# Kernel tuning notes

Measured on AMD Instinct MI355X. Metric: run time of the kernel, lower is better.

The kernel has to match this reference:

```python
import jax, jax.numpy as jnp
import numpy as np

NU, NB, NI = 50000, 20000, 100000
D = 64
NUM_LAYERS = 2
CORE_K = 3
PAD = NI  # padding index for bundle_items
BATCH, NCAND = 2048, 2
MAXDEG = 50
E_UB, E_UI, E_BI = 800000, 1000000, 1200000
N_UB, N_UI, N_BI = NU + NB, NU + NI, NB + NI


def setup_inputs():
    key = jax.random.key(0)
    ks = jax.random.split(key, 24)
    f = jnp.float32
    inp = {
        'users_feature': jax.random.normal(ks[0], (NU, D), f) * 0.1,
        'bundles_feature': jax.random.normal(ks[1], (NB, D), f) * 0.1,
        'items_feature': jax.random.normal(ks[2], (NI, D), f) * 0.1,
        'mlp_core_w1': jax.random.normal(ks[3], (2, 32), f) * 0.1,
        'mlp_core_b1': jnp.zeros((32,), f),
        'mlp_core_w2': jax.random.normal(ks[4], (32, 1), f) * 0.1,
        'mlp_core_b2': jnp.zeros((1,), f),
        'mlp_syn_w1': jax.random.normal(ks[5], (2 * D, D), f) * 0.05,
        'mlp_syn_b1': jnp.zeros((D,), f),
        'mlp_syn_w2': jax.random.normal(ks[6], (D, D), f) * 0.05,
        'mlp_syn_b2': jnp.zeros((D,), f),
        'ub_val': jax.random.uniform(ks[7], (E_UB,), f) * 0.2,
        'ui_val': jax.random.uniform(ks[8], (E_UI,), f) * 0.2,
        'bi_val': jax.random.uniform(ks[9], (E_BI,), f) * 0.2,
        'users': jax.random.randint(ks[10], (BATCH,), 0, NU),
        'bundles': jax.random.randint(ks[11], (BATCH, NCAND), 0, NB),
        'ub_row': jax.random.randint(ks[12], (E_UB,), 0, N_UB, jnp.int32),
        'ub_col': jax.random.randint(ks[13], (E_UB,), 0, N_UB, jnp.int32),
        'ui_row': jax.random.randint(ks[14], (E_UI,), 0, N_UI, jnp.int32),
        'ui_col': jax.random.randint(ks[15], (E_UI,), 0, N_UI, jnp.int32),
        'bi_row': jax.random.randint(ks[16], (E_BI,), 0, N_BI, jnp.int32),
        'bi_col': jax.random.randint(ks[17], (E_BI,), 0, N_BI, jnp.int32),
        'bundle_items': jax.random.randint(ks[18], (NB, MAXDEG), 0, NI + 1),
    }
    return inp


def spmm(row, col, val, x):
    # y = A @ x for COO sparse A: gather source rows, scale, scatter-add to dest rows
    return jax.ops.segment_sum(val[:, None] * x[col], row, num_segments=x.shape[0])


def propagate(row, col, val, feat_a, feat_b):
    f = jnp.concatenate([feat_a, feat_b], axis=0)
    acc = f
    for _ in range(NUM_LAYERS):
        f = spmm(row, col, val, f)
        acc = acc + f
    m = acc / (NUM_LAYERS + 1)  # mean over hop outputs
    return m[:feat_a.shape[0]], m[feat_a.shape[0]:]


def core_fringe_scores(users, bundles, reps, bundle_items,
                       cw1, cb1, cw2, cb2, sw1, sb1, sw2, sb2):
    UB_u, UB_b, UI_u, UI_i, BI_b, BI_i = reps
    B, C = bundles.shape
    users_exp = jnp.repeat(users, C)            # [B*C]
    bundles_flat = bundles.reshape(-1)          # [B*C]
    bbi = bundle_items[bundles_flat]            # [B*C, M]
    mask = bbi != PAD
    zero = jnp.zeros((1, D), UI_i.dtype)
    items_ui = jnp.concatenate([UI_i, zero], 0)[bbi]  # [B*C, M, D]
    items_bi = jnp.concatenate([BI_i, zero], 0)[bbi]
    u_ui = UI_u[users_exp]                      # [B*C, D]
    b_bi = BI_b[bundles_flat]
    r_UI = jnp.einsum('nd,nmd->nm', u_ui, items_ui)
    r_BI = jnp.einsum('nd,nmd->nm', b_bi, items_bi)
    x = jnp.stack([r_UI, r_BI], axis=-1)        # [B*C, M, 2]
    h = jax.nn.relu(x @ cw1 + cb1)              # dropout omitted (eval-mode determinism)
    logits = (h @ cw2 + cb2)[..., 0]
    logits = jnp.where(mask, logits, -jnp.inf)
    pi = jax.nn.softmax(logits, axis=1)
    k = min(CORE_K, bbi.shape[1])
    topv, topi = jax.lax.top_k(pi, k)
    topp = topv / (topv.sum(axis=1, keepdims=True) + 1e-10)
    core_emb = jnp.take_along_axis(items_ui, topi[:, :, None], axis=1)
    h_core = (core_emb * topp[:, :, None]).sum(axis=1)
    n = pi.shape[0]
    is_core = jnp.zeros(pi.shape, bool).at[jnp.arange(n)[:, None], topi].set(True)
    is_fringe = mask & ~is_core
    fr = is_fringe[:, :, None].astype(items_ui.dtype)
    fringe_sum = (items_ui * fr).sum(axis=1)
    fringe_cnt = jnp.maximum(is_fringe.sum(axis=1, keepdims=True).astype(items_ui.dtype), 1.0)
    h_fringe = fringe_sum / fringe_cnt
    syn = jnp.concatenate([h_core, h_fringe], axis=1)
    phi = jax.nn.relu(syn @ sw1 + sb1) @ sw2 + sb2
    hat_e_BI = h_core + phi
    user_final = jnp.concatenate([u_ui, UB_u[users_exp]], axis=1)
    bundle_final = jnp.concatenate([UB_b[bundles_flat], hat_e_BI], axis=1)
    scores = (user_final * bundle_final).sum(axis=1)
    return scores.reshape(B, C)


def reference(users_feature, bundles_feature, items_feature,
              mlp_core_w1, mlp_core_b1, mlp_core_w2, mlp_core_b2,
              mlp_syn_w1, mlp_syn_b1, mlp_syn_w2, mlp_syn_b2,
              ub_val, ui_val, bi_val,
              users, bundles, ub_row, ub_col, ui_row, ui_col,
              bi_row, bi_col, bundle_items):
    UB_u, UB_b = propagate(ub_row, ub_col, ub_val, users_feature, bundles_feature)
    UI_u, UI_i = propagate(ui_row, ui_col, ui_val, users_feature, items_feature)
    BI_b, BI_i = propagate(bi_row, bi_col, bi_val, bundles_feature, items_feature)
    reps = (UB_u, UB_b, UI_u, UI_i, BI_b, BI_i)
    scores = core_fringe_scores(users, bundles, reps, bundle_items,
                                mlp_core_w1, mlp_core_b1, mlp_core_w2, mlp_core_b2,
                                mlp_syn_w1, mlp_syn_b1, mlp_syn_w2, mlp_syn_b2)
    # BPR loss: -log(sigmoid(pos - neg)) == softplus(neg - pos)
    bpr_loss = jnp.mean(jax.nn.softplus(scores[:, 1:] - scores[:, 0:1]))
    return bpr_loss
```

## Files before the change

### kernel.cpp

```cpp
#include <hip/hip_runtime.h>
#include <math.h>

constexpr int D = 64;
constexpr int NU = 50000, NB = 20000, NI = 100000;
constexpr int BATCH = 2048, NCAND = 2, MAXDEG = 50, CORE_K = 3;
constexpr int PAD_IDX = NI;
constexpr int N_UB = NU + NB, N_UI = NU + NI, N_BI = NB + NI;
constexpr int N_TOT = N_UB + N_UI + N_BI;
constexpr int OFF1 = N_UB;
constexpr int OFF2 = N_UB + N_UI;
constexpr int CAP = 48;
constexpr float VAL_SCALE = 16383.0f / 0.2f;
constexpr float VAL_INV   = 0.2f / 16383.0f;

constexpr int GB_BASE = NU;
constexpr int GI_BASE = NU + NB;
constexpr int NGF = NU + NB + NI;

constexpr int BSHIFT = 11;
constexpr int BROWS  = 1 << BSHIFT;
constexpr int NBUCK  = (N_TOT + BROWS - 1) >> BSHIFT;
constexpr int BCAP   = 24576;
constexpr int P1_EPT = 16;
constexpr int P1_TPB = 256;
constexpr int P1_EPB = P1_EPT * P1_TPB;
constexpr int SPLIT  = 4;
constexpr int RWIN   = BROWS / SPLIT;

constexpr int L2_NCB = BATCH * NCAND;
constexpr int L2_SLOTS = 2 * NI + 2 * BATCH + 2 * L2_NCB;
constexpr int S_UBU = 2 * NI;
constexpr int S_UIU = 2 * NI + BATCH;
constexpr int S_UBB = 2 * NI + 2 * BATCH;
constexpr int S_BIB = S_UBB + L2_NCB;

__device__ __forceinline__ float wave_sum64(float v) {
#pragma unroll
    for (int off = 32; off > 0; off >>= 1) v += __shfl_down(v, off);
    return v;
}

__device__ __forceinline__ float bflo(unsigned u) { return __uint_as_float(u << 16); }
__device__ __forceinline__ float bfhi(unsigned u) { return __uint_as_float(u & 0xFFFF0000u); }
__device__ __forceinline__ unsigned short f2bf(float f) {
    unsigned u = __float_as_uint(f);
    u += 0x7FFF + ((u >> 16) & 1);
    return (unsigned short)(u >> 16);
}
__device__ __forceinline__ unsigned pack2(float a, float b) {
    return (unsigned)f2bf(a) | ((unsigned)f2bf(b) << 16);
}
__device__ __forceinline__ float bf1(const unsigned short* p) {
    return __uint_as_float(((unsigned)*p) << 16);
}

__device__ __forceinline__ void edge_decode(unsigned u, int& col, float& v) {
    col = (int)(u & 0x3FFFFu);
    v = (float)(u >> 18) * VAL_INV;
}

__device__ __forceinline__ void gather_rows(const unsigned* __restrict__ ce, int deg,
                                            const unsigned short* __restrict__ src,
                                            int t8, float a[8]) {
    int j = 0;
    for (; j + 3 < deg; j += 4) {
        int c[4]; float v[4]; uint4 u[4];
#pragma unroll
        for (int k = 0; k < 4; ++k) edge_decode(ce[j + k], c[k], v[k]);
#pragma unroll
        for (int k = 0; k < 4; ++k)
            u[k] = *(const uint4*)(src + (((size_t)c[k]) << 6) + t8 * 8);
#pragma unroll
        for (int k = 0; k < 4; ++k) {
            a[0] = fmaf(v[k], bflo(u[k].x), a[0]); a[1] = fmaf(v[k], bfhi(u[k].x), a[1]);
            a[2] = fmaf(v[k], bflo(u[k].y), a[2]); a[3] = fmaf(v[k], bfhi(u[k].y), a[3]);
            a[4] = fmaf(v[k], bflo(u[k].z), a[4]); a[5] = fmaf(v[k], bfhi(u[k].z), a[5]);
            a[6] = fmaf(v[k], bflo(u[k].w), a[6]); a[7] = fmaf(v[k], bfhi(u[k].w), a[7]);
        }
    }
    for (; j < deg; ++j) {
        int c0; float v0;
        edge_decode(ce[j], c0, v0);
        uint4 u0 = *(const uint4*)(src + (((size_t)c0) << 6) + t8 * 8);
        a[0] = fmaf(v0, bflo(u0.x), a[0]); a[1] = fmaf(v0, bfhi(u0.x), a[1]);
        a[2] = fmaf(v0, bflo(u0.y), a[2]); a[3] = fmaf(v0, bfhi(u0.y), a[3]);
        a[4] = fmaf(v0, bflo(u0.z), a[4]); a[5] = fmaf(v0, bfhi(u0.z), a[5]);
        a[6] = fmaf(v0, bflo(u0.w), a[6]); a[7] = fmaf(v0, bfhi(u0.w), a[7]);
    }
}

__global__ __launch_bounds__(256) void k_bin1cvt(
    const int* __restrict__ r0, const int* __restrict__ c0,
    const float* __restrict__ v0,
    const int* __restrict__ r1, const int* __restrict__ c1,
    const float* __restrict__ v1,
    const int* __restrict__ r2, const int* __restrict__ c2,
    const float* __restrict__ v2,
    int e0, int e1, int e2, int nb1,
    int* __restrict__ bcnt, uint2* __restrict__ stage,
    const float* __restrict__ uf, const float* __restrict__ bf,
    const float* __restrict__ itf, unsigned short* __restrict__ gt) {
    const int t = threadIdx.x;
    if ((int)blockIdx.x >= nb1) {
        size_t i = (size_t)(blockIdx.x - nb1) * 256 + t;
        if (i >= (size_t)NGF * 16) return;
        int row = (int)(i >> 4);
        int q = ((int)i & 15) * 4;
        const float* src;
        if (row < GB_BASE)      src = uf  + (size_t)row * D;
        else if (row < GI_BASE) src = bf  + (size_t)(row - GB_BASE) * D;
        else                    src = itf + (size_t)(row - GI_BASE) * D;
        float4 v = *(const float4*)(src + q);
        ushort4 o;
        o.x = f2bf(v.x); o.y = f2bf(v.y); o.z = f2bf(v.z); o.w = f2bf(v.w);
        *(ushort4*)(gt + (size_t)row * D + q) = o;
        return;
    }
    __shared__ int s_hist[NBUCK];
    __shared__ unsigned s_base[NBUCK];
    const int etot = e0 + e1 + e2;
    const int i0 = blockIdx.x * P1_EPB + t;
    if (t < NBUCK) s_hist[t] = 0;
    __syncthreads();
    unsigned el[P1_EPT], er[P1_EPT];
#pragma unroll
    for (int k = 0; k < P1_EPT; ++k) {
        int i = i0 + k * P1_TPB;
        if (i < etot) {
            int r, g; float v;
            if (i < e0)           { r = r0[i]; g = c0[i]; v = v0[i]; }
            else if (i < e0 + e1) { int j = i - e0; r = r1[j] + OFF1;
                                    int c = c1[j]; g = (c < NU) ? c : c + NB; v = v1[j]; }
            else                  { int j = i - e0 - e1; r = r2[j] + OFF2;
                                    g = c2[j] + NU; v = v2[j]; }
            unsigned q = (unsigned)fminf(v * VAL_SCALE + 0.5f, 16383.0f);
            el[k] = (q << 18) | (unsigned)g;
            int lo = atomicAdd(&s_hist[r >> BSHIFT], 1);
            er[k] = (unsigned)r | ((unsigned)lo << 19);
        } else {
            er[k] = 0xFFFFFFFFu;
        }
    }
    __syncthreads();
    if (t < NBUCK) s_base[t] = (unsigned)atomicAdd(&bcnt[t], s_hist[t]);
    __syncthreads();
#pragma unroll
    for (int k = 0; k < P1_EPT; ++k) {
        unsigned eh = er[k];
        if (eh == 0xFFFFFFFFu) continue;
        unsigned r = eh & 0x7FFFFu;
        unsigned b = r >> BSHIFT;
        unsigned slot = s_base[b] + (eh >> 19);
        if (slot < (unsigned)BCAP)
            stage[(size_t)b * BCAP + slot] = make_uint2(el[k], r);
    }
}

__global__ __launch_bounds__(512) void k_bin2l1(
    const int* __restrict__ bcnt, const uint2* __restrict__ stage,
    const unsigned short* __restrict__ gt,
    int* __restrict__ cnt, unsigned* __restrict__ cv,
    unsigned short* __restrict__ y1) {
    __shared__ int s_c[RWIN];
    const int cb = blockIdx.x >> 2;
    const int p  = blockIdx.x & 3;
    const int t  = threadIdx.x;
    const int rb = (cb << BSHIFT) + p * RWIN;
    s_c[t] = 0;
    __syncthreads();
    int nb = bcnt[cb]; if (nb > BCAP) nb = BCAP;
    const uint2* sp = stage + (size_t)cb * BCAP;
    for (int i = t; i < nb; i += 512) {
        uint2 e = sp[i];
        int rl = (int)e.y - rb;
        if ((unsigned)rl < (unsigned)RWIN) {
            int slot = atomicAdd(&s_c[rl], 1);
            if (slot < CAP) cv[(size_t)e.y * CAP + slot] = e.x;
        }
    }
    __syncthreads();
    if (rb + t < N_TOT) cnt[rb + t] = s_c[t];
    const int t8 = t & 7;
#pragma unroll 1
    for (int pass = 0; pass < 8; ++pass) {
        int rl = pass * 64 + (t >> 3);
        int r = rb + rl;
        if (r >= N_TOT) continue;
        int deg = s_c[rl]; if (deg > CAP) deg = CAP;
        float a[8];
#pragma unroll
        for (int k = 0; k < 8; ++k) a[k] = 0.f;
        gather_rows(cv + (size_t)r * CAP, deg, gt, t8, a);
        uint4 o;
        o.x = pack2(a[0], a[1]); o.y = pack2(a[2], a[3]);
        o.z = pack2(a[4], a[5]); o.w = pack2(a[6], a[7]);
        *(uint4*)(y1 + ((size_t)r << 6) + t8 * 8) = o;
    }
}

__global__ __launch_bounds__(256) void k_spmm_l2(
    const int* __restrict__ cnt, const unsigned* __restrict__ cv,
    const int* __restrict__ users, const int* __restrict__ bundles,
    const unsigned short* __restrict__ y1, const unsigned short* __restrict__ gt,
    unsigned short* __restrict__ xc) {
    int s = blockIdx.x * 32 + (threadIdx.x >> 3);
    int t = threadIdx.x & 7;
    if (s >= L2_SLOTS) return;
    int r, g, sec;
    if (s < NI)                { r = OFF1 + NU + s;        g = GI_BASE + s;        sec = 1; }
    else if (s < 2 * NI)       { int i = s - NI;
                                 r = OFF2 + NB + i;        g = GI_BASE + i;        sec = 2; }
    else {
        int q = s - 2 * NI;
        if (q < BATCH)            { int u = users[q];             r = u;         g = u;            sec = 0; }
        else if (q < 2 * BATCH)   { int u = users[q - BATCH];     r = OFF1 + u;  g = u;            sec = 1; }
        else if (q < S_BIB - 2 * NI) { int b = bundles[q - 2 * BATCH];
                                    r = NU + b;    g = GB_BASE + b;  sec = 0; }
        else                      { int b = bundles[q - (S_BIB - 2 * NI)];
                                    r = OFF2 + b;  g = GB_BASE + b;  sec = 2; }
    }
    auto y1row = [&](int gg) -> int {
        if (sec == 0) return gg;
        if (sec == 2) return OFF2 - GB_BASE + gg;
        return OFF1 + ((gg < NU) ? gg : gg - NB);
    };
    int deg = cnt[r]; if (deg > CAP) deg = CAP;
    const unsigned* ce = cv + (size_t)r * CAP;
    float a[8];
#pragma unroll
    for (int k = 0; k < 8; ++k) a[k] = 0.f;
    int j = 0;
    for (; j + 3 < deg; j += 4) {
        int c[4]; float v[4]; uint4 u[4];
#pragma unroll
        for (int k = 0; k < 4; ++k) edge_decode(ce[j + k], c[k], v[k]);
#pragma unroll
        for (int k = 0; k < 4; ++k)
            u[k] = *(const uint4*)(y1 + (((size_t)y1row(c[k])) << 6) + t * 8);
#pragma unroll
        for (int k = 0; k < 4; ++k) {
            a[0] = fmaf(v[k], bflo(u[k].x), a[0]); a[1] = fmaf(v[k], bfhi(u[k].x), a[1]);
            a[2] = fmaf(v[k], bflo(u[k].y), a[2]); a[3] = fmaf(v[k], bfhi(u[k].y), a[3]);
            a[4] = fmaf(v[k], bflo(u[k].z), a[4]); a[5] = fmaf(v[k], bfhi(u[k].z), a[5]);
            a[6] = fmaf(v[k], bflo(u[k].w), a[6]); a[7] = fmaf(v[k], bfhi(u[k].w), a[7]);
        }
    }
    for (; j < deg; ++j) {
        int c0; float v0;
        edge_decode(ce[j], c0, v0);
        uint4 u0 = *(const uint4*)(y1 + (((size_t)y1row(c0)) << 6) + t * 8);
        a[0] = fmaf(v0, bflo(u0.x), a[0]); a[1] = fmaf(v0, bfhi(u0.x), a[1]);
        a[2] = fmaf(v0, bflo(u0.y), a[2]); a[3] = fmaf(v0, bfhi(u0.y), a[3]);
        a[4] = fmaf(v0, bflo(u0.z), a[4]); a[5] = fmaf(v0, bfhi(u0.z), a[5]);
        a[6] = fmaf(v0, bflo(u0.w), a[6]); a[7] = fmaf(v0, bfhi(u0.w), a[7]);
    }
    uint4 fx = *(const uint4*)(gt + ((size_t)g << 6) + t * 8);
    uint4 yx = *(const uint4*)(y1 + ((size_t)r << 6) + t * 8);
    constexpr float k3 = 1.0f / 3.0f;
    float o[8];
    o[0] = (bflo(fx.x) + bflo(yx.x) + a[0]) * k3;
    o[1] = (bfhi(fx.x) + bfhi(yx.x) + a[1]) * k3;
    o[2] = (bflo(fx.y) + bflo(yx.y) + a[2]) * k3;
    o[3] = (bfhi(fx.y) + bfhi(yx.y) + a[3]) * k3;
    o[4] = (bflo(fx.z) + bflo(yx.z) + a[4]) * k3;
    o[5] = (bfhi(fx.z) + bfhi(yx.z) + a[5]) * k3;
    o[6] = (bflo(fx.w) + bflo(yx.w) + a[6]) * k3;
    o[7] = (bfhi(fx.w) + bfhi(yx.w) + a[7]) * k3;
    uint4 w;
    w.x = pack2(o[0], o[1]); w.y = pack2(o[2], o[3]);
    w.z = pack2(o[4], o[5]); w.w = pack2(o[6], o[7]);
    *(uint4*)(xc + ((size_t)s << 6) + t * 8) = w;
}

__global__ __launch_bounds__(256) void k_score(
    const int* __restrict__ bundles,
    const int* __restrict__ bundle_items,
    const unsigned short* __restrict__ xc,
    const float* __restrict__ cw1, const float* __restrict__ cb1,
    const float* __restrict__ cw2, const float* __restrict__ cb2,
    const float* __restrict__ sw1, const float* __restrict__ sb1,
    const float* __restrict__ sw2, const float* __restrict__ sb2,
    float* __restrict__ accum, unsigned* __restrict__ tick,
    float* __restrict__ out) {
    const int t  = threadIdx.x;
    const int wv = t >> 6;
    const int ln = t & 63;
    const int n  = blockIdx.x * 4 + wv;
    const int g8 = ln >> 3;
    const int l8 = ln & 7;
    const int uq = n >> 1;
    const int b = bundles[n];

    __shared__ unsigned sh_it[4][MAXDEG][32];
    __shared__ float sh_r[4][2][MAXDEG];
    __shared__ float sh_syn[4][2 * D];
    __shared__ float sh_h1[4][D];
    __shared__ float sh_sc[4];

    int my_idx = (ln < MAXDEG) ? bundle_items[(size_t)b * MAXDEG + ln] : PAD_IDX;
    unsigned long long vmask = __ballot(my_idx != PAD_IDX);

    uint4 ufr = *(const uint4*)(xc + (((size_t)(S_UIU + uq)) << 6) + l8 * 8);
    uint4 bfr = *(const uint4*)(xc + (((size_t)(S_BIB + n)) << 6) + l8 * 8);
    float uf0 = bflo(ufr.x), uf1 = bfhi(ufr.x), uf2 = bflo(ufr.y), uf3 = bfhi(ufr.y);
    float uf4 = bflo(ufr.z), uf5 = bfhi(ufr.z), uf6 = bflo(ufr.w), uf7 = bfhi(ufr.w);
    float bf0 = bflo(bfr.x), bf1_ = bfhi(bfr.x), bf2 = bflo(bfr.y), bf3 = bfhi(bfr.y);
    float bf4 = bflo(bfr.z), bf5 = bfhi(bfr.z), bf6 = bflo(bfr.w), bf7 = bfhi(bfr.w);

    for (int iter = 0; iter < (MAXDEG + 7) / 8; ++iter) {
        int m = iter * 8 + g8;
        if (m >= MAXDEG) continue;
        int it = __shfl(my_idx, m);
        uint4 iu = make_uint4(0, 0, 0, 0);
        float pu = 0.f, pb = 0.f;
        if (it != PAD_IDX) {
            iu = *(const uint4*)(xc + (((size_t)it) << 6) + l8 * 8);
            uint4 ib = *(const uint4*)(xc + (((size_t)(NI + it)) << 6) + l8 * 8);
            pu = uf0 * bflo(iu.x) + uf1 * bfhi(iu.x) + uf2 * bflo(iu.y) + uf3 * bfhi(iu.y)
               + uf4 * bflo(iu.z) + uf5 * bfhi(iu.z) + uf6 * bflo(iu.w) + uf7 * bfhi(iu.w);
            pb = bf0 * bflo(ib.x) + bf1_ * bfhi(ib.x) + bf2 * bflo(ib.y) + bf3 * bfhi(ib.y)
               + bf4 * bflo(ib.z) + bf5 * bfhi(ib.z) + bf6 * bflo(ib.w) + bf7 * bfhi(ib.w);
        }
        *(uint4*)&sh_it[wv][m][l8 * 4] = iu;
#pragma unroll
        for (int off = 4; off > 0; off >>= 1) {
            pu += __shfl_down(pu, off, 8);
            pb += __shfl_down(pb, off, 8);
        }
        if (l8 == 0) { sh_r[wv][0][m] = pu; sh_r[wv][1][m] = pb; }
    }
    __builtin_amdgcn_wave_barrier();

    float logit = -INFINITY;
    if (ln < MAXDEG && my_idx != PAD_IDX) {
        float rU = sh_r[wv][0][ln], rB = sh_r[wv][1][ln];
        float acc = cb2[0];
#pragma unroll
        for (int j = 0; j < 32; ++j) {
            float h = fmaf(rU, cw1[j], fmaf(rB, cw1[32 + j], cb1[j]));
            h = fmaxf(h, 0.f);
            acc = fmaf(h, cw2[j], acc);
        }
        logit = acc;
    }

    float mx = logit;
#pragma unroll
    for (int off = 32; off > 0; off >>= 1) mx = fmaxf(mx, __shfl_xor(mx, off));
    float e = expf(logit - mx);
    float sm = e;
#pragma unroll
    for (int off = 32; off > 0; off >>= 1) sm += __shfl_xor(sm, off);
    float p = e / sm;

    int ti[CORE_K]; float tp[CORE_K];
    float vsel = p;
#pragma unroll
    for (int k = 0; k < CORE_K; ++k) {
        float vv = vsel; int ii = ln;
#pragma unroll
        for (int off = 32; off > 0; off >>= 1) {
            float v2 = __shfl_xor(vv, off);
            int   i2 = __shfl_xor(ii, off);
            if (v2 > vv || (v2 == vv && i2 < ii)) { vv = v2; ii = i2; }
        }
        ti[k] = ii; tp[k] = vv;
        if (ln == ii) vsel = -1.f;
    }
    float tinv = 1.f / (tp[0] + tp[1] + tp[2] + 1e-10f);
    tp[0] *= tinv; tp[1] *= tinv; tp[2] *= tinv;

    int ti0 = ti[0], ti1 = ti[1], ti2 = ti[2];
    const int ui_w = ln >> 1;
    const bool hi = (ln & 1);
    auto feat = [&](int m) -> float {
        unsigned w = sh_it[wv][m][ui_w];
        return hi ? bfhi(w) : bflo(w);
    };
    float hcore = feat(ti0) * tp[0] + feat(ti1) * tp[1] + feat(ti2) * tp[2];
    float fsum = 0.f;
#pragma unroll 10
    for (int m = 0; m < MAXDEG; ++m) fsum += feat(m);
    int fcnt = __popcll(vmask);
#pragma unroll
    for (int k = 0; k < CORE_K; ++k) {
        if ((vmask >> ti[k]) & 1ull) { fsum -= feat(ti[k]); fcnt--; }
    }
    float hfr = fsum / fmaxf((float)fcnt, 1.f);
    sh_syn[wv][ln] = hcore;
    sh_syn[wv][D + ln] = hfr;
    __builtin_amdgcn_wave_barrier();

    float h1 = sb1[ln];
#pragma unroll 8
    for (int k0 = 0; k0 < 32; ++k0) {
        float4 s4 = *(const float4*)&sh_syn[wv][k0 * 4];
        h1 = fmaf(s4.x, sw1[(k0 * 4 + 0) * D + ln], h1);
        h1 = fmaf(s4.y, sw1[(k0 * 4 + 1) * D + ln], h1);
        h1 = fmaf(s4.z, sw1[(k0 * 4 + 2) * D + ln], h1);
        h1 = fmaf(s4.w, sw1[(k0 * 4 + 3) * D + ln], h1);
    }
    sh_h1[wv][ln] = fmaxf(h1, 0.f);
    __builtin_amdgcn_wave_barrier();
    float phi = sb2[ln];
#pragma unroll 8
    for (int k0 = 0; k0 < 16; ++k0) {
        float4 s4 = *(const float4*)&sh_h1[wv][k0 * 4];
        phi = fmaf(s4.x, sw2[(k0 * 4 + 0) * D + ln], phi);
        phi = fmaf(s4.y, sw2[(k0 * 4 + 1) * D + ln], phi);
        phi = fmaf(s4.z, sw2[(k0 * 4 + 2) * D + ln], phi);
        phi = fmaf(s4.w, sw2[(k0 * 4 + 3) * D + ln], phi);
    }

    float hat = hcore + phi;
    float uui = bf1(xc + (((size_t)(S_UIU + uq)) << 6) + ln);
    float ubu = bf1(xc + (((size_t)(S_UBU + uq)) << 6) + ln);
    float ubb = bf1(xc + (((size_t)(S_UBB + n)) << 6) + ln);
    float part = wave_sum64(uui * ubb + ubu * hat);
    if (ln == 0) sh_sc[wv] = part;

    __syncthreads();
    if (t == 0) {
        float x01 = sh_sc[1] - sh_sc[0];
        float x23 = sh_sc[3] - sh_sc[2];
        float spv = fmaxf(x01, 0.f) + log1pf(expf(-fabsf(x01)))
                  + fmaxf(x23, 0.f) + log1pf(expf(-fabsf(x23)));
        atomicAdd(accum, spv * (1.0f / (float)BATCH));
        __threadfence();
        unsigned old = atomicAdd(tick, 1u);
        if (old == gridDim.x - 1) {
            __threadfence();
            float total = atomicAdd(accum, 0.0f);
            out[0] = total;
        }
    }
}

extern "C" void kernel_launch(void* const* d_in, const int* in_sizes, int n_in,
                              void* d_out, int out_size, void* d_ws, size_t ws_size,
                              hipStream_t stream) {
    const float* users_feature   = (const float*)d_in[0];
    const float* bundles_feature = (const float*)d_in[1];
    const float* items_feature   = (const float*)d_in[2];
    const float* cw1 = (const float*)d_in[3];
    const float* cb1 = (const float*)d_in[4];
    const float* cw2 = (const float*)d_in[5];
    const float* cb2 = (const float*)d_in[6];
    const float* sw1 = (const float*)d_in[7];
    const float* sb1 = (const float*)d_in[8];
    const float* sw2 = (const float*)d_in[9];
    const float* sb2 = (const float*)d_in[10];
    const float* ub_val = (const float*)d_in[11];
    const float* ui_val = (const float*)d_in[12];
    const float* bi_val = (const float*)d_in[13];
    const int* users   = (const int*)d_in[14];
    const int* bundles = (const int*)d_in[15];
    const int* ub_row = (const int*)d_in[16];
    const int* ub_col = (const int*)d_in[17];
    const int* ui_row = (const int*)d_in[18];
    const int* ui_col = (const int*)d_in[19];
    const int* bi_row = (const int*)d_in[20];
    const int* bi_col = (const int*)d_in[21];
    const int* bundle_items = (const int*)d_in[22];
    const int E_UB = in_sizes[11], E_UI = in_sizes[12], E_BI = in_sizes[13];
    const int E_TOT = E_UB + E_UI + E_BI;

    float* ws = (float*)d_ws;
    size_t off = 0;
    unsigned short* gt  = (unsigned short*)(ws + off); off += (size_t)NGF * 32;
    unsigned short* y1b = (unsigned short*)(ws + off); off += (size_t)N_TOT * 32;
    unsigned* cv  = (unsigned*)(ws + off); off += (size_t)N_TOT * CAP;
    uint2* stage = (uint2*)(ws + off);
    unsigned short* xc = (unsigned short*)(ws + off);
    off += (size_t)NBUCK * BCAP * 2;
    int*   cnt    = (int*)(ws + off); off += N_TOT;
    int*   bcnt   = (int*)(ws + off); off += NBUCK;
    unsigned* tick = (unsigned*)(ws + off); off += 1;
    float* accum  = (float*)(ws + off); off += 1;
    if (ws_size < off * sizeof(float)) return;

    hipMemsetAsync(bcnt, 0, (NBUCK + 2) * sizeof(int), stream);

    const int nb1 = (E_TOT + P1_EPB - 1) / P1_EPB;
    const int ncvt = (int)(((size_t)NGF * 16 + 255) / 256);
    k_bin1cvt<<<nb1 + ncvt, P1_TPB, 0, stream>>>(
        ub_row, ub_col, ub_val, ui_row, ui_col, ui_val, bi_row, bi_col, bi_val,
        E_UB, E_UI, E_BI, nb1, bcnt, stage,
        users_feature, bundles_feature, items_feature, gt);

    k_bin2l1<<<NBUCK * SPLIT, 512, 0, stream>>>(bcnt, stage, gt, cnt, cv, y1b);

    k_spmm_l2<<<(L2_SLOTS + 31) / 32, 256, 0, stream>>>(
        cnt, cv, users, bundles, y1b, gt, xc);

    k_score<<<(BATCH * NCAND) / 4, 256, 0, stream>>>(
        bundles, bundle_items, xc,
        cw1, cb1, cw2, cb2, sw1, sb1, sw2, sb2,
        accum, tick, (float*)d_out);
}
```

Baseline: 381.4 us.

## Split bucket scatter from layer-1 SpMM and halve bucket size

Separates the second binning pass from the first-layer SpMM gather into two kernels. Binning now uses one block per bucket of 1024 rows, so each staged edge is read once instead of by four split blocks. The layer-1 SpMM runs as its own row-parallel kernel with many more blocks, which should improve latency hiding for the gathers. The cost is an extra kernel launch and re-reading cnt from global memory. More buckets also mean more global atomics in the first pass.

```diff
diff --git a/kernel.cpp b/kernel.cpp
--- a/kernel.cpp
+++ b/kernel.cpp
@@ -17,15 +17,13 @@
 constexpr int GI_BASE = NU + NB;
 constexpr int NGF = NU + NB + NI;
 
-constexpr int BSHIFT = 11;
+constexpr int BSHIFT = 10;
 constexpr int BROWS  = 1 << BSHIFT;
 constexpr int NBUCK  = (N_TOT + BROWS - 1) >> BSHIFT;
-constexpr int BCAP   = 24576;
+constexpr int BCAP   = 12288;
 constexpr int P1_EPT = 16;
 constexpr int P1_TPB = 256;
 constexpr int P1_EPB = P1_EPT * P1_TPB;
-constexpr int SPLIT  = 4;
-constexpr int RWIN   = BROWS / SPLIT;
 
 constexpr int L2_NCB = BATCH * NCAND;
 constexpr int L2_SLOTS = 2 * NI + 2 * BATCH + 2 * L2_NCB;
@@ -57,36 +55,6 @@
 __device__ __forceinline__ void edge_decode(unsigned u, int& col, float& v) {
     col = (int)(u & 0x3FFFFu);
     v = (float)(u >> 18) * VAL_INV;
-}
-
-__device__ __forceinline__ void gather_rows(const unsigned* __restrict__ ce, int deg,
-                                            const unsigned short* __restrict__ src,
-                                            int t8, float a[8]) {
-    int j = 0;
-    for (; j + 3 < deg; j += 4) {
-        int c[4]; float v[4]; uint4 u[4];
-#pragma unroll
-        for (int k = 0; k < 4; ++k) edge_decode(ce[j + k], c[k], v[k]);
-#pragma unroll
-        for (int k = 0; k < 4; ++k)
-            u[k] = *(const uint4*)(src + (((size_t)c[k]) << 6) + t8 * 8);
-#pragma unroll
-        for (int k = 0; k < 4; ++k) {
-            a[0] = fmaf(v[k], bflo(u[k].x), a[0]); a[1] = fmaf(v[k], bfhi(u[k].x), a[1]);
-            a[2] = fmaf(v[k], bflo(u[k].y), a[2]); a[3] = fmaf(v[k], bfhi(u[k].y), a[3]);
-            a[4] = fmaf(v[k], bflo(u[k].z), a[4]); a[5] = fmaf(v[k], bfhi(u[k].z), a[5]);
-            a[6] = fmaf(v[k], bflo(u[k].w), a[6]); a[7] = fmaf(v[k], bfhi(u[k].w), a[7]);
-        }
-    }
-    for (; j < deg; ++j) {
-        int c0; float v0;
-        edge_decode(ce[j], c0, v0);
-        uint4 u0 = *(const uint4*)(src + (((size_t)c0) << 6) + t8 * 8);
-        a[0] = fmaf(v0, bflo(u0.x), a[0]); a[1] = fmaf(v0, bfhi(u0.x), a[1]);
-        a[2] = fmaf(v0, bflo(u0.y), a[2]); a[3] = fmaf(v0, bfhi(u0.y), a[3]);
-        a[4] = fmaf(v0, bflo(u0.z), a[4]); a[5] = fmaf(v0, bfhi(u0.z), a[5]);
-        a[6] = fmaf(v0, bflo(u0.w), a[6]); a[7] = fmaf(v0, bfhi(u0.w), a[7]);
-    }
 }
 
 __global__ __launch_bounds__(256) void k_bin1cvt(
@@ -120,7 +88,7 @@
     __shared__ unsigned s_base[NBUCK];
     const int etot = e0 + e1 + e2;
     const int i0 = blockIdx.x * P1_EPB + t;
-    if (t < NBUCK) s_hist[t] = 0;
+    for (int l = t; l < NBUCK; l += P1_TPB) s_hist[l] = 0;
     __syncthreads();
     unsigned el[P1_EPT], er[P1_EPT];
 #pragma unroll
@@ -142,7 +110,8 @@
         }
     }
     __syncthreads();
-    if (t < NBUCK) s_base[t] = (unsigned)atomicAdd(&bcnt[t], s_hist[t]);
+    for (int l = t; l < NBUCK; l += P1_TPB)
+        s_base[l] = (unsigned)atomicAdd(&bcnt[l], s_hist[l]);
     __syncthreads();
 #pragma unroll
     for (int k = 0; k < P1_EPT; ++k) {
@@ -156,46 +125,69 @@
     }
 }
 
-__global__ __launch_bounds__(512) void k_bin2l1(
+__global__ __launch_bounds__(512) void k_bin2(
     const int* __restrict__ bcnt, const uint2* __restrict__ stage,
-    const unsigned short* __restrict__ gt,
-    int* __restrict__ cnt, unsigned* __restrict__ cv,
-    unsigned short* __restrict__ y1) {
-    __shared__ int s_c[RWIN];
-    const int cb = blockIdx.x >> 2;
-    const int p  = blockIdx.x & 3;
-    const int t  = threadIdx.x;
-    const int rb = (cb << BSHIFT) + p * RWIN;
-    s_c[t] = 0;
-    __syncthreads();
-    int nb = bcnt[cb]; if (nb > BCAP) nb = BCAP;
-    const uint2* sp = stage + (size_t)cb * BCAP;
+    int* __restrict__ cnt, unsigned* __restrict__ cv) {
+    __shared__ int s_c[BROWS];
+    const int b = blockIdx.x;
+    const int t = threadIdx.x;
+    for (int l = t; l < BROWS; l += 512) s_c[l] = 0;
+    __syncthreads();
+    int nb = bcnt[b]; if (nb > BCAP) nb = BCAP;
+    const uint2* sp = stage + (size_t)b * BCAP;
+    const int rbase = b << BSHIFT;
     for (int i = t; i < nb; i += 512) {
         uint2 e = sp[i];
-        int rl = (int)e.y - rb;
-        if ((unsigned)rl < (unsigned)RWIN) {
-            int slot = atomicAdd(&s_c[rl], 1);
-            if (slot < CAP) cv[(size_t)e.y * CAP + slot] = e.x;
-        }
-    }
-    __syncthreads();
-    if (rb + t < N_TOT) cnt[rb + t] = s_c[t];
-    const int t8 = t & 7;
-#pragma unroll 1
-    for (int pass = 0; pass < 8; ++pass) {
-        int rl = pass * 64 + (t >> 3);
-        int r = rb + rl;
-        if (r >= N_TOT) continue;
-        int deg = s_c[rl]; if (deg > CAP) deg = CAP;
-        float a[8];
-#pragma unroll
-        for (int k = 0; k < 8; ++k) a[k] = 0.f;
-        gather_rows(cv + (size_t)r * CAP, deg, gt, t8, a);
-        uint4 o;
-        o.x = pack2(a[0], a[1]); o.y = pack2(a[2], a[3]);
-        o.z = pack2(a[4], a[5]); o.w = pack2(a[6], a[7]);
-        *(uint4*)(y1 + ((size_t)r << 6) + t8 * 8) = o;
-    }
+        int slot = atomicAdd(&s_c[(int)e.y - rbase], 1);
+        if (slot < CAP) cv[(size_t)e.y * CAP + slot] = e.x;
+    }
+    __syncthreads();
+    for (int l = t; l < BROWS; l += 512) {
+        int r = rbase + l;
+        if (r < N_TOT) cnt[r] = s_c[l];
+    }
+}
+
+__global__ __launch_bounds__(256) void k_spmm_l1(
+    const int* __restrict__ cnt, const unsigned* __restrict__ cv,
+    const unsigned short* __restrict__ gt, unsigned short* __restrict__ y1) {
+    int r = blockIdx.x * 32 + (threadIdx.x >> 3);
+    int t = threadIdx.x & 7;
+    if (r >= N_TOT) return;
+    int deg = cnt[r]; if (deg > CAP) deg = CAP;
+    const unsigned* ce = cv + (size_t)r * CAP;
+    float a[8];
+#pragma unroll
+    for (int k = 0; k < 8; ++k) a[k] = 0.f;
+    int j = 0;
+    for (; j + 3 < deg; j += 4) {
+        int c[4]; float v[4]; uint4 u[4];
+#pragma unroll
+        for (int k = 0; k < 4; ++k) edge_decode(ce[j + k], c[k], v[k]);
+#pragma unroll
+        for (int k = 0; k < 4; ++k)
+            u[k] = *(const uint4*)(gt + (((size_t)c[k]) << 6) + t * 8);
+#pragma unroll
+        for (int k = 0; k < 4; ++k) {
+            a[0] = fmaf(v[k], bflo(u[k].x), a[0]); a[1] = fmaf(v[k], bfhi(u[k].x), a[1]);
+            a[2] = fmaf(v[k], bflo(u[k].y), a[2]); a[3] = fmaf(v[k], bfhi(u[k].y), a[3]);
+            a[4] = fmaf(v[k], bflo(u[k].z), a[4]); a[5] = fmaf(v[k], bfhi(u[k].z), a[5]);
+            a[6] = fmaf(v[k], bflo(u[k].w), a[6]); a[7] = fmaf(v[k], bfhi(u[k].w), a[7]);
+        }
+    }
+    for (; j < deg; ++j) {
+        int c0; float v0;
+        edge_decode(ce[j], c0, v0);
+        uint4 u0 = *(const uint4*)(gt + (((size_t)c0) << 6) + t * 8);
+        a[0] = fmaf(v0, bflo(u0.x), a[0]); a[1] = fmaf(v0, bfhi(u0.x), a[1]);
+        a[2] = fmaf(v0, bflo(u0.y), a[2]); a[3] = fmaf(v0, bfhi(u0.y), a[3]);
+        a[4] = fmaf(v0, bflo(u0.z), a[4]); a[5] = fmaf(v0, bfhi(u0.z), a[5]);
+        a[6] = fmaf(v0, bflo(u0.w), a[6]); a[7] = fmaf(v0, bfhi(u0.w), a[7]);
+    }
+    uint4 o;
+    o.x = pack2(a[0], a[1]); o.y = pack2(a[2], a[3]);
+    o.z = pack2(a[4], a[5]); o.w = pack2(a[6], a[7]);
+    *(uint4*)(y1 + ((size_t)r << 6) + t * 8) = o;
 }
 
 __global__ __launch_bounds__(256) void k_spmm_l2(
@@ -488,7 +480,9 @@
         E_UB, E_UI, E_BI, nb1, bcnt, stage,
         users_feature, bundles_feature, items_feature, gt);
 
-    k_bin2l1<<<NBUCK * SPLIT, 512, 0, stream>>>(bcnt, stage, gt, cnt, cv, y1b);
+    k_bin2<<<NBUCK, 512, 0, stream>>>(bcnt, stage, cnt, cv);
+
+    k_spmm_l1<<<(N_TOT + 31) / 32, 256, 0, stream>>>(cnt, cv, gt, y1b);
 
     k_spmm_l2<<<(L2_SLOTS + 31) / 32, 256, 0, stream>>>(
         cnt, cv, users, bundles, y1b, gt, xc);
```

After: 366.6 us. 3.9% less time.
